# Kernel tuning notes

Hardware: AMD Instinct MI355X
Metric: run time of the kernel (lower is better)

Reference implementation:

```python
import jax, jax.numpy as jnp
import numpy as np

HRANGE = 8192


def setup_inputs() -> dict:
    key = jax.random.key(0)
    k_hs, k_start, k_end, k_cores = jax.random.split(key, 4)
    B, n_chunks, dim, rank = 16384, 4, 64, 16
    hs = jax.random.randint(k_hs, (B, n_chunks), 0, HRANGE, dtype=jnp.int64)
    # init scales from reset_parameters: cores/end ~ U(-r^-0.5, r^-0.5), start ~ U(-d^-0.5, d^-0.5)
    start_core = jax.random.uniform(k_start, (HRANGE, dim, rank), jnp.float32, -dim ** -0.5, dim ** -0.5)
    end_core = jax.random.uniform(k_end, (HRANGE, dim, rank), jnp.float32, -rank ** -0.5, rank ** -0.5)
    cores = jax.random.uniform(k_cores, (n_chunks - 2, HRANGE, dim, rank, rank), jnp.float32, -rank ** -0.5, rank ** -0.5)
    return {"hs": hs, "start_core": start_core, "end_core": end_core, "cores": cores}


def reference(hs, start_core, end_core, cores):
    # hs: [B, n_chunks] hashed indices; tensor-train matrix-chain contraction.
    v = end_core[hs[:, -1]]  # [B, d, r]
    n_mid = cores.shape[0]  # n_chunks - 2 (small, structural loop)
    for i in range(n_mid):
        ci = cores[i][hs[:, i + 1]]  # [B, d, r, s] gathered core slices
        v = jnp.einsum('bdrs,bdr->bds', ci, v)
    return jnp.einsum('bdr,bdr->bd', start_core[hs[:, 0]], v)  # [B, d]
```

## Files before the change

kernel.cpp:

```cpp
#include <hip/hip_runtime.h>

#define HRANGE 8192
#define DIM 64
#define RANK 16
#define CAP 64


typedef float floatx4 __attribute__((ext_vector_type(4)));

__device__ __forceinline__ void fma4(float4& a, float s, const float4& m) {
    a.x = fmaf(s, m.x, a.x); a.y = fmaf(s, m.y, a.y);
    a.z = fmaf(s, m.z, a.z); a.w = fmaf(s, m.w, a.w);
}
__device__ __forceinline__ float4 ld4(const float* p) {
    return *reinterpret_cast<const float4*>(p);
}
__device__ __forceinline__ float4 ldnt4(const float* p) {
    floatx4 t = __builtin_nontemporal_load(reinterpret_cast<const floatx4*>(p));
    return make_float4(t.x, t.y, t.z, t.w);
}
__device__ __forceinline__ unsigned short f2bf(float x) {
    unsigned int u = __float_as_uint(x);
    u += 0x7FFFu + ((u >> 16) & 1u);
    return (unsigned short)(u >> 16);
}
__device__ __forceinline__ float blo(unsigned int u) { return __uint_as_float(u << 16); }
__device__ __forceinline__ float bhi(unsigned int u) { return __uint_as_float(u & 0xFFFF0000u); }

__global__ __launch_bounds__(256) void zero_kernel(int* p, int n) {
    int i = blockIdx.x * blockDim.x + threadIdx.x;
    if (i < n) p[i] = 0;
}

__global__ __launch_bounds__(256) void bin_kernel(const int* __restrict__ hs,
                                                  int* hist1, int* hist2,
                                                  int* ovfc, int* nec,
                                                  int* wl1, int* wl2,
                                                  int* list1, int* list2,
                                                  int* ovf1, int* ovf2, int B) {
    int b = blockIdx.x * blockDim.x + threadIdx.x;
    if (b >= B) return;
    int h1 = hs[b * 4 + 1];
    int s1 = atomicAdd(&hist1[h1], 1);
    if (s1 == 0) { int w = atomicAdd(&nec[0], 1); wl1[w] = h1; }
    if (s1 < CAP) list1[h1 * CAP + s1] = b;
    else { int o = atomicAdd(&ovfc[0], 1); ovf1[o] = b; }
    int h2 = hs[b * 4 + 2];
    int s2 = atomicAdd(&hist2[h2], 1);
    if (s2 == 0) { int w = atomicAdd(&nec[1], 1); wl2[w] = h2; }
    if (s2 < CAP) list2[h2 * CAP + s2] = b;
    else { int o = atomicAdd(&ovfc[1], 1); ovf2[o] = b; }
}

__global__ __launch_bounds__(64) void pass1_kernel(const int* __restrict__ hs,
                                                   const float* __restrict__ end_core,
                                                   const float* __restrict__ cores0,
                                                   const int* __restrict__ hist1,
                                                   const int* __restrict__ list1,
                                                   const int* __restrict__ nec,
                                                   const int* __restrict__ wl1,
                                                   const int* __restrict__ ovfc,
                                                   const int* __restrict__ ovf1,
                                                   unsigned short* __restrict__ v1) {
    const int lane = threadIdx.x;
    const int dl = lane >> 2, q = lane & 3;
    const int bid = blockIdx.x;

    if (bid < HRANGE * 4) {
        const int widx = bid >> 2;
        if (widx >= nec[0]) return;
        const int h = wl1[widx];
        const int d = (bid & 3) * 16 + dl;

        const float* Mrow = cores0 + ((size_t)h * DIM + d) * (RANK * RANK) + q * 4;
        float4 M[16];
        #pragma unroll
        for (int r = 0; r < 16; ++r) M[r] = ldnt4(Mrow + r * RANK);

        const int cnt = hist1[h];
        const int n = cnt < CAP ? cnt : CAP;

        __shared__ int sb[CAP], sh[CAP];
        if (lane < n) {
            int b = list1[h * CAP + lane];
            sb[lane] = b;
            sh[lane] = hs[b * 4 + 3];
        }
        __syncthreads();

        float4 n0, n1, n2, n3;
        { const float* e = end_core + ((size_t)sh[0] * DIM + d) * RANK;
          n0 = ld4(e); n1 = ld4(e + 4); n2 = ld4(e + 8); n3 = ld4(e + 12); }
        for (int i = 0; i < n; ++i) {
            float4 c0 = n0, c1 = n1, c2 = n2, c3 = n3;
            if (i + 1 < n) {
                const float* e = end_core + ((size_t)sh[i + 1] * DIM + d) * RANK;
                n0 = ld4(e); n1 = ld4(e + 4); n2 = ld4(e + 8); n3 = ld4(e + 12);
            }
            float4 acc = make_float4(0.f, 0.f, 0.f, 0.f);
            fma4(acc, c0.x, M[0]);  fma4(acc, c0.y, M[1]);
            fma4(acc, c0.z, M[2]);  fma4(acc, c0.w, M[3]);
            fma4(acc, c1.x, M[4]);  fma4(acc, c1.y, M[5]);
            fma4(acc, c1.z, M[6]);  fma4(acc, c1.w, M[7]);
            fma4(acc, c2.x, M[8]);  fma4(acc, c2.y, M[9]);
            fma4(acc, c2.z, M[10]); fma4(acc, c2.w, M[11]);
            fma4(acc, c3.x, M[12]); fma4(acc, c3.y, M[13]);
            fma4(acc, c3.z, M[14]); fma4(acc, c3.w, M[15]);
            *reinterpret_cast<ushort4*>(v1 + (size_t)sb[i] * (DIM * RANK) + d * RANK + q * 4) =
                make_ushort4(f2bf(acc.x), f2bf(acc.y), f2bf(acc.z), f2bf(acc.w));
        }
    } else {
        const int d = (bid - HRANGE * 4) * 16 + dl;
        const int no = ovfc[0];
        for (int i = 0; i < no; ++i) {
            int b = ovf1[i];
            int h = hs[b * 4 + 1], h3 = hs[b * 4 + 3];
            const float* Mrow = cores0 + ((size_t)h * DIM + d) * (RANK * RANK) + q * 4;
            const float* e = end_core + ((size_t)h3 * DIM + d) * RANK;
            float4 e0 = ld4(e), e1 = ld4(e + 4), e2 = ld4(e + 8), e3 = ld4(e + 12);
            const float ev[16] = {e0.x, e0.y, e0.z, e0.w, e1.x, e1.y, e1.z, e1.w,
                                  e2.x, e2.y, e2.z, e2.w, e3.x, e3.y, e3.z, e3.w};
            float4 acc = make_float4(0.f, 0.f, 0.f, 0.f);
            #pragma unroll
            for (int r = 0; r < 16; ++r) fma4(acc, ev[r], ld4(Mrow + r * RANK));
            *reinterpret_cast<ushort4*>(v1 + (size_t)b * (DIM * RANK) + d * RANK + q * 4) =
                make_ushort4(f2bf(acc.x), f2bf(acc.y), f2bf(acc.z), f2bf(acc.w));
        }
    }
}

__global__ __launch_bounds__(64) void pass2_kernel(const int* __restrict__ hs,
                                                   const float* __restrict__ start_core,
                                                   const float* __restrict__ cores1,
                                                   const int* __restrict__ hist2,
                                                   const int* __restrict__ list2,
                                                   const int* __restrict__ nec,
                                                   const int* __restrict__ wl2,
                                                   const int* __restrict__ ovfc,
                                                   const int* __restrict__ ovf2,
                                                   const unsigned short* __restrict__ v1,
                                                   float* __restrict__ out) {
    const int lane = threadIdx.x;
    const int dl = lane >> 2, q = lane & 3;
    const int bid = blockIdx.x;

    if (bid < HRANGE * 4) {
        const int widx = bid >> 2;
        if (widx >= nec[0]) return;
        const int h = wl2[widx];
        const int d = (bid & 3) * 16 + dl;

        const float* Mrow = cores1 + ((size_t)h * DIM + d) * (RANK * RANK) + q * 4;
        float4 M[16];
        #pragma unroll
        for (int r = 0; r < 16; ++r) M[r] = ldnt4(Mrow + r * RANK);

        const int cnt = hist2[h];
        const int n = cnt < CAP ? cnt : CAP;

        __shared__ int sb[CAP], sh0[CAP];
        if (lane < n) {
            int b = list2[h * CAP + lane];
            sb[lane] = b;
            sh0[lane] = hs[b * 4 + 0];
        }
        __syncthreads();

        uint4 na, nb; float4 nsc;
        { const unsigned short* vv = v1 + (size_t)sb[0] * (DIM * RANK) + d * RANK;
          na = *reinterpret_cast<const uint4*>(vv);
          nb = *reinterpret_cast<const uint4*>(vv + 8);
          nsc = ld4(start_core + ((size_t)sh0[0] * DIM + d) * RANK + q * 4); }
        for (int i = 0; i < n; ++i) {
            uint4 a = na, bb = nb; float4 sc = nsc;
            if (i + 1 < n) {
                const unsigned short* vv = v1 + (size_t)sb[i + 1] * (DIM * RANK) + d * RANK;
                na = *reinterpret_cast<const uint4*>(vv);
                nb = *reinterpret_cast<const uint4*>(vv + 8);
                nsc = ld4(start_core + ((size_t)sh0[i + 1] * DIM + d) * RANK + q * 4);
            }
            float4 c0 = make_float4(blo(a.x),  bhi(a.x),  blo(a.y),  bhi(a.y));
            float4 c1 = make_float4(blo(a.z),  bhi(a.z),  blo(a.w),  bhi(a.w));
            float4 c2 = make_float4(blo(bb.x), bhi(bb.x), blo(bb.y), bhi(bb.y));
            float4 c3 = make_float4(blo(bb.z), bhi(bb.z), blo(bb.w), bhi(bb.w));
            float4 acc = make_float4(0.f, 0.f, 0.f, 0.f);
            fma4(acc, c0.x, M[0]);  fma4(acc, c0.y, M[1]);
            fma4(acc, c0.z, M[2]);  fma4(acc, c0.w, M[3]);
            fma4(acc, c1.x, M[4]);  fma4(acc, c1.y, M[5]);
            fma4(acc, c1.z, M[6]);  fma4(acc, c1.w, M[7]);
            fma4(acc, c2.x, M[8]);  fma4(acc, c2.y, M[9]);
            fma4(acc, c2.z, M[10]); fma4(acc, c2.w, M[11]);
            fma4(acc, c3.x, M[12]); fma4(acc, c3.y, M[13]);
            fma4(acc, c3.z, M[14]); fma4(acc, c3.w, M[15]);
            float partial = acc.x * sc.x + acc.y * sc.y + acc.z * sc.z + acc.w * sc.w;
            partial += __shfl_xor(partial, 1);
            partial += __shfl_xor(partial, 2);
            if (q == 0) out[(size_t)sb[i] * DIM + d] = partial;
        }
    } else {
        const int d = (bid - HRANGE * 4) * 16 + dl;
        const int no = ovfc[0];
        for (int i = 0; i < no; ++i) {
            int b = ovf2[i];
            int h = hs[b * 4 + 2], h0 = hs[b * 4 + 0];
            const float* Mrow = cores1 + ((size_t)h * DIM + d) * (RANK * RANK) + q * 4;
            const unsigned short* vv = v1 + (size_t)b * (DIM * RANK) + d * RANK;
            uint4 a = *reinterpret_cast<const uint4*>(vv);
            uint4 bb = *reinterpret_cast<const uint4*>(vv + 8);
            const float ev[16] = {blo(a.x),  bhi(a.x),  blo(a.y),  bhi(a.y),
                                  blo(a.z),  bhi(a.z),  blo(a.w),  bhi(a.w),
                                  blo(bb.x), bhi(bb.x), blo(bb.y), bhi(bb.y),
                                  blo(bb.z), bhi(bb.z), blo(bb.w), bhi(bb.w)};
            float4 acc = make_float4(0.f, 0.f, 0.f, 0.f);
            #pragma unroll
            for (int r = 0; r < 16; ++r) fma4(acc, ev[r], ld4(Mrow + r * RANK));
            float4 sc = ld4(start_core + ((size_t)h0 * DIM + d) * RANK + q * 4);
            float partial = acc.x * sc.x + acc.y * sc.y + acc.z * sc.z + acc.w * sc.w;
            partial += __shfl_xor(partial, 1);
            partial += __shfl_xor(partial, 2);
            if (q == 0) out[(size_t)b * DIM + d] = partial;
        }
    }
}

extern "C" void kernel_launch(void* const* d_in, const int* in_sizes, int n_in,
                              void* d_out, int out_size, void* d_ws, size_t ws_size,
                              hipStream_t stream) {
    const int*   hs         = (const int*)d_in[0];
    const float* start_core = (const float*)d_in[1];
    const float* end_core   = (const float*)d_in[2];
    const float* cores      = (const float*)d_in[3];
    float*       out        = (float*)d_out;
    const int B = in_sizes[0] / 4;

    unsigned short* v1 = (unsigned short*)d_ws;
    int* hist1 = (int*)(v1 + (size_t)B * DIM * RANK);
    int* hist2 = hist1 + HRANGE;
    int* ovfc  = hist2 + HRANGE;
    int* nec   = ovfc + 2;
    int* wl1   = nec + 2;
    int* wl2   = wl1 + HRANGE;
    int* list1 = wl2 + HRANGE;
    int* list2 = list1 + HRANGE * CAP;
    int* ovf1  = list2 + HRANGE * CAP;
    int* ovf2  = ovf1 + B;

    zero_kernel<<<(2 * HRANGE + 4 + 255) / 256, 256, 0, stream>>>(hist1, 2 * HRANGE + 4);
    bin_kernel<<<(B + 255) / 256, 256, 0, stream>>>(hs, hist1, hist2, ovfc, nec,
                                                    wl1, wl2, list1, list2, ovf1, ovf2, B);
    pass1_kernel<<<HRANGE * 4 + 4, 64, 0, stream>>>(hs, end_core, cores,
                                                    hist1, list1, nec, wl1, ovfc, ovf1, v1);
    pass2_kernel<<<HRANGE * 4 + 4, 64, 0, stream>>>(hs, start_core,
                                                    cores + (size_t)HRANGE * DIM * RANK * RANK,
                                                    hist2, list2, nec + 1, wl2, ovfc + 1, ovf2,
                                                    v1, out);
}
```

Before: 230.3 us.

## Merge four d-slice blocks into one 256-thread block with LDS-staged vectors

Each hash bucket is now handled by a single 256-thread block covering all 64 d rows instead of four 64-thread blocks. Per-sample end_core and v1 rows are loaded cooperatively and fully coalesced into a padded, double-buffered shared-memory tile, and each thread then reads its row from LDS. The bucket list and index loads are shared across the whole block rather than repeated four times. The zero kernel is replaced with hipMemsetAsync. In exchange, the per-iteration loop now has a block-wide barrier, and the block has fewer independent waves to hide latency.

```diff
diff --git a/kernel.cpp b/kernel.cpp
--- a/kernel.cpp
+++ b/kernel.cpp
@@ -26,11 +26,6 @@
 }
 __device__ __forceinline__ float blo(unsigned int u) { return __uint_as_float(u << 16); }
 __device__ __forceinline__ float bhi(unsigned int u) { return __uint_as_float(u & 0xFFFF0000u); }
-
-__global__ __launch_bounds__(256) void zero_kernel(int* p, int n) {
-    int i = blockIdx.x * blockDim.x + threadIdx.x;
-    if (i < n) p[i] = 0;
-}
 
 __global__ __launch_bounds__(256) void bin_kernel(const int* __restrict__ hs,
                                                   int* hist1, int* hist2,
@@ -52,25 +47,24 @@
     else { int o = atomicAdd(&ovfc[1], 1); ovf2[o] = b; }
 }
 
-__global__ __launch_bounds__(64) void pass1_kernel(const int* __restrict__ hs,
-                                                   const float* __restrict__ end_core,
-                                                   const float* __restrict__ cores0,
-                                                   const int* __restrict__ hist1,
-                                                   const int* __restrict__ list1,
-                                                   const int* __restrict__ nec,
-                                                   const int* __restrict__ wl1,
-                                                   const int* __restrict__ ovfc,
-                                                   const int* __restrict__ ovf1,
-                                                   unsigned short* __restrict__ v1) {
-    const int lane = threadIdx.x;
-    const int dl = lane >> 2, q = lane & 3;
+__global__ __launch_bounds__(256) void pass1_kernel(const int* __restrict__ hs,
+                                                    const float* __restrict__ end_core,
+                                                    const float* __restrict__ cores0,
+                                                    const int* __restrict__ hist1,
+                                                    const int* __restrict__ list1,
+                                                    const int* __restrict__ nec,
+                                                    const int* __restrict__ wl1,
+                                                    const int* __restrict__ ovfc,
+                                                    const int* __restrict__ ovf1,
+                                                    unsigned short* __restrict__ v1) {
+    const int t = threadIdx.x;
+    const int dl = (t >> 2) & 15, q = t & 3, w = t >> 6;
+    const int d = w * 16 + dl;
     const int bid = blockIdx.x;
 
-    if (bid < HRANGE * 4) {
-        const int widx = bid >> 2;
-        if (widx >= nec[0]) return;
-        const int h = wl1[widx];
-        const int d = (bid & 3) * 16 + dl;
+    if (bid < HRANGE) {
+        if (bid >= nec[0]) return;
+        const int h = wl1[bid];
 
         const float* Mrow = cores0 + ((size_t)h * DIM + d) * (RANK * RANK) + q * 4;
         float4 M[16];
@@ -81,22 +75,26 @@
         const int n = cnt < CAP ? cnt : CAP;
 
         __shared__ int sb[CAP], sh[CAP];
-        if (lane < n) {
-            int b = list1[h * CAP + lane];
-            sb[lane] = b;
-            sh[lane] = hs[b * 4 + 3];
+        __shared__ float ebuf[2][1280];
+        if (t < n) {
+            int b = list1[h * CAP + t];
+            sb[t] = b;
+            sh[t] = hs[b * 4 + 3];
         }
         __syncthreads();
 
-        float4 n0, n1, n2, n3;
-        { const float* e = end_core + ((size_t)sh[0] * DIM + d) * RANK;
-          n0 = ld4(e); n1 = ld4(e + 4); n2 = ld4(e + 8); n3 = ld4(e + 12); }
+        {
+            const float* e = end_core + (size_t)sh[0] * (DIM * RANK);
+            *reinterpret_cast<float4*>(&ebuf[0][(t >> 2) * 20 + (t & 3) * 4]) = ld4(e + t * 4);
+        }
         for (int i = 0; i < n; ++i) {
-            float4 c0 = n0, c1 = n1, c2 = n2, c3 = n3;
+            __syncthreads();
             if (i + 1 < n) {
-                const float* e = end_core + ((size_t)sh[i + 1] * DIM + d) * RANK;
-                n0 = ld4(e); n1 = ld4(e + 4); n2 = ld4(e + 8); n3 = ld4(e + 12);
+                const float* e = end_core + (size_t)sh[i + 1] * (DIM * RANK);
+                *reinterpret_cast<float4*>(&ebuf[(i + 1) & 1][(t >> 2) * 20 + (t & 3) * 4]) = ld4(e + t * 4);
             }
+            const float* eb = &ebuf[i & 1][d * 20];
+            float4 c0 = ld4(eb), c1 = ld4(eb + 4), c2 = ld4(eb + 8), c3 = ld4(eb + 12);
             float4 acc = make_float4(0.f, 0.f, 0.f, 0.f);
             fma4(acc, c0.x, M[0]);  fma4(acc, c0.y, M[1]);
             fma4(acc, c0.z, M[2]);  fma4(acc, c0.w, M[3]);
@@ -110,45 +108,43 @@
                 make_ushort4(f2bf(acc.x), f2bf(acc.y), f2bf(acc.z), f2bf(acc.w));
         }
     } else {
-        const int d = (bid - HRANGE * 4) * 16 + dl;
         const int no = ovfc[0];
         for (int i = 0; i < no; ++i) {
             int b = ovf1[i];
             int h = hs[b * 4 + 1], h3 = hs[b * 4 + 3];
-            const float* Mrow = cores0 + ((size_t)h * DIM + d) * (RANK * RANK) + q * 4;
+            const float* Mr = cores0 + ((size_t)h * DIM + d) * (RANK * RANK) + q * 4;
             const float* e = end_core + ((size_t)h3 * DIM + d) * RANK;
             float4 e0 = ld4(e), e1 = ld4(e + 4), e2 = ld4(e + 8), e3 = ld4(e + 12);
             const float ev[16] = {e0.x, e0.y, e0.z, e0.w, e1.x, e1.y, e1.z, e1.w,
                                   e2.x, e2.y, e2.z, e2.w, e3.x, e3.y, e3.z, e3.w};
             float4 acc = make_float4(0.f, 0.f, 0.f, 0.f);
             #pragma unroll
-            for (int r = 0; r < 16; ++r) fma4(acc, ev[r], ld4(Mrow + r * RANK));
+            for (int r = 0; r < 16; ++r) fma4(acc, ev[r], ld4(Mr + r * RANK));
             *reinterpret_cast<ushort4*>(v1 + (size_t)b * (DIM * RANK) + d * RANK + q * 4) =
                 make_ushort4(f2bf(acc.x), f2bf(acc.y), f2bf(acc.z), f2bf(acc.w));
         }
     }
 }
 
-__global__ __launch_bounds__(64) void pass2_kernel(const int* __restrict__ hs,
-                                                   const float* __restrict__ start_core,
-                                                   const float* __restrict__ cores1,
-                                                   const int* __restrict__ hist2,
-                                                   const int* __restrict__ list2,
-                                                   const int* __restrict__ nec,
-                                                   const int* __restrict__ wl2,
-                                                   const int* __restrict__ ovfc,
-                                                   const int* __restrict__ ovf2,
-                                                   const unsigned short* __restrict__ v1,
-                                                   float* __restrict__ out) {
-    const int lane = threadIdx.x;
-    const int dl = lane >> 2, q = lane & 3;
+__global__ __launch_bounds__(256) void pass2_kernel(const int* __restrict__ hs,
+                                                    const float* __restrict__ start_core,
+                                                    const float* __restrict__ cores1,
+                                                    const int* __restrict__ hist2,
+                                                    const int* __restrict__ list2,
+                                                    const int* __restrict__ nec,
+                                                    const int* __restrict__ wl2,
+                                                    const int* __restrict__ ovfc,
+                                                    const int* __restrict__ ovf2,
+                                                    const unsigned short* __restrict__ v1,
+                                                    float* __restrict__ out) {
+    const int t = threadIdx.x;
+    const int dl = (t >> 2) & 15, q = t & 3, w = t >> 6;
+    const int d = w * 16 + dl;
     const int bid = blockIdx.x;
 
-    if (bid < HRANGE * 4) {
-        const int widx = bid >> 2;
-        if (widx >= nec[0]) return;
-        const int h = wl2[widx];
-        const int d = (bid & 3) * 16 + dl;
+    if (bid < HRANGE) {
+        if (bid >= nec[0]) return;
+        const int h = wl2[bid];
 
         const float* Mrow = cores1 + ((size_t)h * DIM + d) * (RANK * RANK) + q * 4;
         float4 M[16];
@@ -159,26 +155,36 @@
         const int n = cnt < CAP ? cnt : CAP;
 
         __shared__ int sb[CAP], sh0[CAP];
-        if (lane < n) {
-            int b = list2[h * CAP + lane];
-            sb[lane] = b;
-            sh0[lane] = hs[b * 4 + 0];
+        __shared__ unsigned int vbuf[2][768];
+        if (t < n) {
+            int b = list2[h * CAP + t];
+            sb[t] = b;
+            sh0[t] = hs[b * 4 + 0];
         }
         __syncthreads();
 
-        uint4 na, nb; float4 nsc;
-        { const unsigned short* vv = v1 + (size_t)sb[0] * (DIM * RANK) + d * RANK;
-          na = *reinterpret_cast<const uint4*>(vv);
-          nb = *reinterpret_cast<const uint4*>(vv + 8);
-          nsc = ld4(start_core + ((size_t)sh0[0] * DIM + d) * RANK + q * 4); }
+        {
+            const unsigned int* vr = reinterpret_cast<const unsigned int*>(
+                v1 + (size_t)sb[0] * (DIM * RANK));
+            *reinterpret_cast<uint2*>(&vbuf[0][(t >> 2) * 12 + (t & 3) * 2]) =
+                *reinterpret_cast<const uint2*>(vr + t * 2);
+        }
+        float4 nsc = ld4(start_core + (size_t)sh0[0] * (DIM * RANK) + t * 4);
         for (int i = 0; i < n; ++i) {
-            uint4 a = na, bb = nb; float4 sc = nsc;
+            __syncthreads();
             if (i + 1 < n) {
-                const unsigned short* vv = v1 + (size_t)sb[i + 1] * (DIM * RANK) + d * RANK;
-                na = *reinterpret_cast<const uint4*>(vv);
-                nb = *reinterpret_cast<const uint4*>(vv + 8);
-                nsc = ld4(start_core + ((size_t)sh0[i + 1] * DIM + d) * RANK + q * 4);
+                const unsigned int* vr = reinterpret_cast<const unsigned int*>(
+                    v1 + (size_t)sb[i + 1] * (DIM * RANK));
+                *reinterpret_cast<uint2*>(&vbuf[(i + 1) & 1][(t >> 2) * 12 + (t & 3) * 2]) =
+                    *reinterpret_cast<const uint2*>(vr + t * 2);
             }
+            float4 sc = nsc;
+            if (i + 1 < n)
+                nsc = ld4(start_core + (size_t)sh0[i + 1] * (DIM * RANK) + t * 4);
+
+            const unsigned int* vb = &vbuf[i & 1][d * 12];
+            uint4 a  = *reinterpret_cast<const uint4*>(vb);
+            uint4 bb = *reinterpret_cast<const uint4*>(vb + 4);
             float4 c0 = make_float4(blo(a.x),  bhi(a.x),  blo(a.y),  bhi(a.y));
             float4 c1 = make_float4(blo(a.z),  bhi(a.z),  blo(a.w),  bhi(a.w));
             float4 c2 = make_float4(blo(bb.x), bhi(bb.x), blo(bb.y), bhi(bb.y));
@@ -198,14 +204,13 @@
             if (q == 0) out[(size_t)sb[i] * DIM + d] = partial;
         }
     } else {
-        const int d = (bid - HRANGE * 4) * 16 + dl;
         const int no = ovfc[0];
         for (int i = 0; i < no; ++i) {
             int b = ovf2[i];
             int h = hs[b * 4 + 2], h0 = hs[b * 4 + 0];
-            const float* Mrow = cores1 + ((size_t)h * DIM + d) * (RANK * RANK) + q * 4;
+            const float* Mr = cores1 + ((size_t)h * DIM + d) * (RANK * RANK) + q * 4;
             const unsigned short* vv = v1 + (size_t)b * (DIM * RANK) + d * RANK;
-            uint4 a = *reinterpret_cast<const uint4*>(vv);
+            uint4 a  = *reinterpret_cast<const uint4*>(vv);
             uint4 bb = *reinterpret_cast<const uint4*>(vv + 8);
             const float ev[16] = {blo(a.x),  bhi(a.x),  blo(a.y),  bhi(a.y),
                                   blo(a.z),  bhi(a.z),  blo(a.w),  bhi(a.w),
@@ -213,7 +218,7 @@
                                   blo(bb.z), bhi(bb.z), blo(bb.w), bhi(bb.w)};
             float4 acc = make_float4(0.f, 0.f, 0.f, 0.f);
             #pragma unroll
-            for (int r = 0; r < 16; ++r) fma4(acc, ev[r], ld4(Mrow + r * RANK));
+            for (int r = 0; r < 16; ++r) fma4(acc, ev[r], ld4(Mr + r * RANK));
             float4 sc = ld4(start_core + ((size_t)h0 * DIM + d) * RANK + q * 4);
             float partial = acc.x * sc.x + acc.y * sc.y + acc.z * sc.z + acc.w * sc.w;
             partial += __shfl_xor(partial, 1);
@@ -245,13 +250,13 @@
     int* ovf1  = list2 + HRANGE * CAP;
     int* ovf2  = ovf1 + B;
 
-    zero_kernel<<<(2 * HRANGE + 4 + 255) / 256, 256, 0, stream>>>(hist1, 2 * HRANGE + 4);
+    hipMemsetAsync(hist1, 0, (2 * HRANGE + 4) * sizeof(int), stream);
     bin_kernel<<<(B + 255) / 256, 256, 0, stream>>>(hs, hist1, hist2, ovfc, nec,
                                                     wl1, wl2, list1, list2, ovf1, ovf2, B);
-    pass1_kernel<<<HRANGE * 4 + 4, 64, 0, stream>>>(hs, end_core, cores,
-                                                    hist1, list1, nec, wl1, ovfc, ovf1, v1);
-    pass2_kernel<<<HRANGE * 4 + 4, 64, 0, stream>>>(hs, start_core,
-                                                    cores + (size_t)HRANGE * DIM * RANK * RANK,
-                                                    hist2, list2, nec + 1, wl2, ovfc + 1, ovf2,
-                                                    v1, out);
-}
+    pass1_kernel<<<HRANGE + 1, 256, 0, stream>>>(hs, end_core, cores,
+                                                 hist1, list1, nec, wl1, ovfc, ovf1, v1);
+    pass2_kernel<<<HRANGE + 1, 256, 0, stream>>>(hs, start_core,
+                                                 cores + (size_t)HRANGE * DIM * RANK * RANK,
+                                                 hist2, list2, nec + 1, wl2, ovfc + 1, ovf2,
+                                                 v1, out);
+}
```

New measurement: 239.1 us. 1.04x slower.
